# Kernel tuning notes

Measured on AMD Instinct MI355X. Metric: run time of the kernel, lower is better.

## Reference

```python
import jax, jax.numpy as jnp
import numpy as np

T, B, D, H, L = 512, 128, 400, 400, 3


def setup_inputs() -> dict:
    key = jax.random.key(0)
    ks = jax.random.split(key, 12)
    x = jax.random.normal(ks[0], (T, B, D), dtype=jnp.float32)
    lengths = jnp.sort(jax.random.randint(ks[1], (B,), 1, T + 1))[::-1]
    s = 1.0 / np.sqrt(H)
    def w(k, shape):
        return jax.random.normal(k, shape, dtype=jnp.float32) * s
    return {
        "x": x,
        "lengths": lengths,
        # forward-direction cells: layer0 input D, layers 1..2 input 2H
        "Wih_f0": w(ks[2], (4 * H, D)),
        "Wih_f12": w(ks[3], (L - 1, 4 * H, 2 * H)),
        "Whh_f": w(ks[4], (L, 4 * H, H)),
        "b_f": jnp.zeros((L, 4 * H), jnp.float32),
        # backward-direction cells
        "Wih_b0": w(ks[5], (4 * H, D)),
        "Wih_b12": w(ks[6], (L - 1, 4 * H, 2 * H)),
        "Whh_b": w(ks[7], (L, 4 * H, H)),
        "b_b": jnp.zeros((L, 4 * H), jnp.float32),
    }


def _layer(x, mask, Wih, Whh, bias, reverse):
    # x: [T,B,Din], mask: [T,B] bool. Precompute input-side gates once.
    gx = jnp.einsum("tbd,gd->tbg", x, Wih) + bias  # [T,B,4H]
    nb, h_dim = x.shape[1], Whh.shape[-1]

    def step(carry, inp):
        h, c = carry
        g_x, m = inp
        g = g_x + h @ Whh.T
        i, f, gc, o = jnp.split(g, 4, axis=-1)
        i, f, o = jax.nn.sigmoid(i), jax.nn.sigmoid(f), jax.nn.sigmoid(o)
        gc = jnp.tanh(gc)
        c_new = f * c + i * gc
        h_new = o * jnp.tanh(c_new)
        m = m[:, None]
        # inactive sequences keep old state (fwd) / init zeros (bwd) -- matches packed semantics
        h = jnp.where(m, h_new, h)
        c = jnp.where(m, c_new, c)
        return (h, c), h

    if reverse:
        gx, m_seq = gx[::-1], mask[::-1]
    else:
        m_seq = mask
    init = (jnp.zeros((nb, h_dim), x.dtype), jnp.zeros((nb, h_dim), x.dtype))
    _, out = jax.lax.scan(step, init, (gx, m_seq))
    if reverse:
        out = out[::-1]
    return out * mask[:, :, None]


def reference(x, lengths, Wih_f0, Wih_f12, Whh_f, b_f, Wih_b0, Wih_b12, Whh_b, b_b):
    mask = jnp.arange(x.shape[0])[:, None] < lengths[None, :]  # [T,B]
    Wih_fs = [Wih_f0, Wih_f12[0], Wih_f12[1]]
    Wih_bs = [Wih_b0, Wih_b12[0], Wih_b12[1]]
    for l in range(L):
        f = _layer(x, mask, Wih_fs[l], Whh_f[l], b_f[l], reverse=False)
        b = _layer(x, mask, Wih_bs[l], Whh_b[l], b_b[l], reverse=True)
        x = jnp.concatenate([f, b], axis=-1)  # [T,B,2H]
    return x
```

## Files before the change

kernel.cpp:

```cpp
#include <hip/hip_runtime.h>
#include <stdint.h>
#include <stddef.h>

#define T_ 512
#define B_ 128
#define D_ 400
#define H_ 400
#define HP 416
#define GP 1664
#define NW 3328
#define K0P 448
#define K12P 832
#define NTILES 13
#define NGRP 8
#define REC_BLOCKS 208
#define PAIRS 208

#define GC_FSTRIDE 576

#define HBT_U64   ((size_t)16*2*16*PAIRS)
#define HBT_BYTES (HBT_U64*8)

#define WHHR_US8  ((size_t)2*13*4*2*13*64)
#define WHHR_BYTES (WHHR_US8*8*2)

typedef __attribute__((ext_vector_type(8))) __bf16 bf16x8;
typedef __attribute__((ext_vector_type(4))) float f32x4;
typedef __attribute__((ext_vector_type(8))) unsigned short us8;

__device__ __forceinline__ unsigned short f2bf(float f){
  unsigned u = __builtin_bit_cast(unsigned, f);
  u = (u + 0x7FFFu + ((u >> 16) & 1u)) >> 16;
  return (unsigned short)u;
}
__device__ __forceinline__ float bf2f(unsigned short s){
  unsigned u = ((unsigned)s) << 16;
  return __builtin_bit_cast(float, u);
}
__device__ __forceinline__ float sigm(float x){ return 1.f / (1.f + __expf(-x)); }
__device__ __forceinline__ float tanh_f(float x){
  float ax = fabsf(x);
  float e = __expf(-2.f * ax);
  float t = (1.f - e) / (1.f + e);
  return x < 0.f ? -t : t;
}
__device__ __forceinline__ void store_gx(float* p, float v){ *p = v; }
__device__ __forceinline__ void store_gx(unsigned short* p, float v){ *p = f2bf(v); }

__device__ __forceinline__ void h_store_u64(unsigned long long* p, unsigned long long v){
  __hip_atomic_store(p, v, __ATOMIC_RELAXED, __HIP_MEMORY_SCOPE_AGENT);
}
__device__ __forceinline__ unsigned long long h_load_u64(const unsigned long long* p){
  return __hip_atomic_load(p, __ATOMIC_RELAXED, __HIP_MEMORY_SCOPE_AGENT);
}

__global__ void k_conv_x0(const float* __restrict__ x, unsigned short* __restrict__ xa){
  const size_t i = (size_t)blockIdx.x*256 + threadIdx.x;
  if (i >= (size_t)T_*B_*K0P) return;
  const int k = (int)(i % K0P);
  const size_t tb = i / K0P;
  xa[i] = f2bf(k < D_ ? x[tb*D_ + k] : 0.f);
}

__global__ void k_prep_wih(const float* __restrict__ wf, const float* __restrict__ wb,
                           int K, int mode, unsigned short* __restrict__ dst){
  const size_t i = (size_t)blockIdx.x*256 + threadIdx.x;
  if (i >= (size_t)NW*K) return;
  const int k = (int)(i % K);
  const int n = (int)(i / K);
  const int d = n / GP, ng = n % GP, g = ng / HP, r = ng % HP;
  const float* Wsrc = d ? wb : wf;
  float v = 0.f;
  if (r < H_){
    if (mode == 0){
      if (k < D_) v = Wsrc[(size_t)(g*H_ + r)*D_ + k];
    } else {
      int ks = (k < 400) ? k : ((k >= 416 && k < 816) ? (k - 16) : -1);
      if (ks >= 0) v = Wsrc[(size_t)(g*H_ + r)*800 + ks];
    }
  }
  dst[i] = f2bf(v);
}

__global__ void k_prep_whhR(const float* __restrict__ wf, const float* __restrict__ wb,
                            unsigned short* __restrict__ dst){
  const size_t i = (size_t)blockIdx.x*256 + threadIdx.x;
  if (i >= WHHR_US8) return;
  const int lane = (int)(i & 63);
  size_t q = i >> 6;
  const int kk = (int)(q % 13); q /= 13;
  const int ch = (int)(q % 2);  q /= 2;
  const int w  = (int)(q % 4);  q /= 4;
  const int tile = (int)(q % 13);
  const int dirx = (int)(q / 13);
  const int c  = tile*32 + ch*16 + (lane & 15);
  const int k0 = kk*32 + (lane >> 4)*8;
  const float* W = dirx ? wb : wf;
  unsigned short v[8];
  #pragma unroll
  for (int e = 0; e < 8; ++e){
    const int k = k0 + e;
    const float x = (c < H_ && k < H_) ? W[(size_t)(w*H_ + c)*H_ + k] : 0.f;
    v[e] = f2bf(x);
  }
  *(us8*)(dst + i*8) = *(const us8*)v;
}

__global__ void k_prep_bias(const float* __restrict__ bsf, const float* __restrict__ bsb,
                            float* __restrict__ dst){
  const int n = blockIdx.x*256 + threadIdx.x;
  if (n >= NW) return;
  const int d = n / GP, ng = n % GP, g = ng / HP, r = ng % HP;
  dst[n] = (r < H_) ? (d ? bsb : bsf)[g*H_ + r] : 0.f;
}

template<typename GXT>
__global__ __launch_bounds__(256) void gemm_gx(
    const unsigned short* __restrict__ X, int lda, int K,
    const unsigned short* __restrict__ W,
    const float* __restrict__ bias,
    GXT* __restrict__ gx,
    const int* __restrict__ lens)
{
  const int t = blockIdx.y;
  if (t >= lens[0]) return;
  const int n0 = blockIdx.x * 128;
  __shared__ unsigned short As[128*64];
  __shared__ unsigned short Bs[128*64];
  const int tid = threadIdx.x;
  const int l = tid & 63;
  const int w = tid >> 6;
  const int wm = (w >> 1) * 64, wn = (w & 1) * 64;
  const int lr = l & 15, lk = l >> 4;
  f32x4 acc[4][4];
  #pragma unroll
  for (int i = 0; i < 4; ++i)
    #pragma unroll
    for (int j = 0; j < 4; ++j) acc[i][j] = (f32x4){0.f,0.f,0.f,0.f};

  const unsigned short* Xb = X + (size_t)t * B_ * lda;
  const int r_ = tid >> 3, s_ = (tid & 7) * 8;

  for (int k0 = 0; k0 < K; k0 += 64){
    us8 va[4], vb[4];
    #pragma unroll
    for (int i = 0; i < 4; ++i){
      const int r = i*32 + r_;
      va[i] = *(const us8*)(Xb + (size_t)r*lda + k0 + s_);
      vb[i] = *(const us8*)(W  + (size_t)(n0 + r)*K + k0 + s_);
    }
    __syncthreads();
    #pragma unroll
    for (int i = 0; i < 4; ++i){
      const int r = i*32 + r_;
      *(us8*)&As[r*64 + s_] = va[i];
      *(us8*)&Bs[r*64 + s_] = vb[i];
    }
    __syncthreads();
    #pragma unroll
    for (int kk = 0; kk < 2; ++kk){
      bf16x8 af[4], bfr[4];
      #pragma unroll
      for (int mi = 0; mi < 4; ++mi)
        af[mi] = __builtin_bit_cast(bf16x8, *(const us8*)&As[(wm + mi*16 + lr)*64 + kk*32 + lk*8]);
      #pragma unroll
      for (int ni = 0; ni < 4; ++ni)
        bfr[ni] = __builtin_bit_cast(bf16x8, *(const us8*)&Bs[(wn + ni*16 + lr)*64 + kk*32 + lk*8]);
      #pragma unroll
      for (int mi = 0; mi < 4; ++mi)
        #pragma unroll
        for (int ni = 0; ni < 4; ++ni)
          acc[mi][ni] = __builtin_amdgcn_mfma_f32_16x16x32_bf16(af[mi], bfr[ni], acc[mi][ni], 0, 0, 0);
    }
  }
  #pragma unroll
  for (int ni = 0; ni < 4; ++ni){
    const int col = n0 + wn + ni*16 + lr;
    const float bv = bias[col];
    #pragma unroll
    for (int mi = 0; mi < 4; ++mi){
      #pragma unroll
      for (int r = 0; r < 4; ++r){
        const int b = wm + mi*16 + lk*4 + r;
        store_gx(gx + ((size_t)t*B_ + b)*NW + col, acc[mi][ni][r] + bv);
      }
    }
  }
}

template<typename GXT, bool LAST>
__global__ __launch_bounds__(256, 1) void lstm_rec(
    const GXT* __restrict__ gx,
    const unsigned short* __restrict__ whhR,
    const int* __restrict__ lens,
    unsigned long long* hbt,
    unsigned short* __restrict__ xn,
    float* __restrict__ out)
{
  __shared__ unsigned short HS[16*424];
  __shared__ float GC[4*GC_FSTRIDE];
  __shared__ float GXS[16*132];

  const int tid = threadIdx.x;
  const int bid = blockIdx.x;
  const int dir  = bid / 104;
  const int rem  = bid % 104;
  const int grp  = rem / NTILES;
  const int tile = rem % NTILES;
  const int l  = tid & 63;
  const int w  = tid >> 6;
  const int lr = l & 15;
  const int lk = l >> 4;
  const int cid = dir*NGRP + grp;

  us8 Bf0[13], Bf1[13];
  {
    const unsigned short* bs =
        whhR + ((size_t)((dir*13 + tile)*4 + w)*2*13*64 + l)*8;
    #pragma unroll
    for (int kk = 0; kk < 13; ++kk)
      Bf0[kk] = *(const us8*)(bs + (size_t)kk*512);
    const unsigned short* bs1 = bs + (size_t)13*64*8;
    #pragma unroll
    for (int kk = 0; kk < 13; ++kk)
      Bf1[kk] = *(const us8*)(bs1 + (size_t)kk*512);
  }
  const int grp_len = lens[grp*16];
  const int eb  = tid & 15;
  const int p2  = tid >> 4;
  const int mylen = lens[grp*16 + eb];
  float cs0 = 0.f, cs1 = 0.f, hs0 = 0.f, hs1 = 0.f;
  __syncthreads();

  int s_a = 0;
  const int pb = tid >> 4, q = tid & 15, qg = q >> 2, qj = (q & 3) * 8;
  unsigned long long* const myslot =
      hbt + (((size_t)cid*2)*16 + eb)*PAIRS + tile*16 + p2;

  for (int s = 0; s < T_; ++s){
    const int t = dir ? (T_ - 1 - s) : s;
    if (t >= grp_len) continue;

    f32x4 pfa, pfb;
    {
      const size_t goff = ((size_t)t*B_ + grp*16 + pb) * NW + (size_t)dir*GP + qg*HP + tile*32 + qj;
      if constexpr (sizeof(GXT) == 4){
        const float* gp = (const float*)gx + goff;
        pfa = *(const f32x4*)gp;
        pfb = *(const f32x4*)(gp + 4);
      } else {
        us8 v = *(const us8*)((const unsigned short*)gx + goff);
        pfa = (f32x4){bf2f(v[0]), bf2f(v[1]), bf2f(v[2]), bf2f(v[3])};
        pfb = (f32x4){bf2f(v[4]), bf2f(v[5]), bf2f(v[6]), bf2f(v[7])};
      }
    }

    {
      const unsigned rtag = (unsigned)s_a;
      const unsigned long long* hb =
          hbt + ((size_t)(cid*2 + (s_a & 1))*16)*PAIRS;
      unsigned long long v[13];
      #pragma unroll
      for (int j = 0; j < 13; ++j)
        v[j] = h_load_u64(hb + j*256 + tid);
      unsigned stale = 0;
      #pragma unroll
      for (int j = 0; j < 13; ++j)
        if ((unsigned)(v[j] >> 32) != rtag) stale |= 1u << j;
      while (stale){
        const unsigned m = stale;
        #pragma unroll
        for (int j = 0; j < 13; ++j)
          if (m & (1u << j)) v[j] = h_load_u64(hb + j*256 + tid);
        #pragma unroll
        for (int j = 0; j < 13; ++j)
          if ((m & (1u << j)) && (unsigned)(v[j] >> 32) == rtag) stale &= ~(1u << j);
      }
      #pragma unroll
      for (int j = 0; j < 13; ++j){
        const int idx = j*256 + tid;
        const int b = idx / PAIRS, p = idx % PAIRS;
        *(unsigned*)&HS[b*424 + 2*p] = (unsigned)v[j];
      }
    }
    __syncthreads();

    f32x4 a0 = (f32x4){0.f,0.f,0.f,0.f}, a1 = (f32x4){0.f,0.f,0.f,0.f};
    {
      const int ab = lr*424 + lk*8;
      #pragma unroll
      for (int kk = 0; kk < 13; ++kk){
        bf16x8 av = __builtin_bit_cast(bf16x8, *(const us8*)&HS[ab + kk*32]);
        a0 = __builtin_amdgcn_mfma_f32_16x16x32_bf16(av, Bf0[kk], a0, 0, 0, 0);
        a1 = __builtin_amdgcn_mfma_f32_16x16x32_bf16(av, Bf1[kk], a1, 0, 0, 0);
      }
    }
    {
      float* Gw = GC + w * GC_FSTRIDE;
      #pragma unroll
      for (int r = 0; r < 4; ++r){
        Gw[(lk*4 + r)*36 + lr]      = a0[r];
        Gw[(lk*4 + r)*36 + 16 + lr] = a1[r];
      }
      float* gp = GXS + pb*132 + qg*32 + qj;
      *(f32x4*)gp = pfa;
      *(f32x4*)(gp + 4) = pfb;
    }
    __syncthreads();

    const bool act = t < mylen;
    const int c0 = 2*p2, c1 = 2*p2 + 1;
    {
      const float gi0 = GC[0*GC_FSTRIDE + eb*36 + c0] + GXS[eb*132 + c0];
      const float gf0 = GC[1*GC_FSTRIDE + eb*36 + c0] + GXS[eb*132 + 32 + c0];
      const float gg0 = GC[2*GC_FSTRIDE + eb*36 + c0] + GXS[eb*132 + 64 + c0];
      const float go0 = GC[3*GC_FSTRIDE + eb*36 + c0] + GXS[eb*132 + 96 + c0];
      const float gi1 = GC[0*GC_FSTRIDE + eb*36 + c1] + GXS[eb*132 + c1];
      const float gf1 = GC[1*GC_FSTRIDE + eb*36 + c1] + GXS[eb*132 + 32 + c1];
      const float gg1 = GC[2*GC_FSTRIDE + eb*36 + c1] + GXS[eb*132 + 64 + c1];
      const float go1 = GC[3*GC_FSTRIDE + eb*36 + c1] + GXS[eb*132 + 96 + c1];
      const float cn0 = sigm(gf0)*cs0 + sigm(gi0)*tanh_f(gg0);
      const float hn0 = sigm(go0) * tanh_f(cn0);
      const float cn1 = sigm(gf1)*cs1 + sigm(gi1)*tanh_f(gg1);
      const float hn1 = sigm(go1) * tanh_f(cn1);
      if (act){ cs0 = cn0; hs0 = hn0; cs1 = cn1; hs1 = hn1; }
    }
    {
      const unsigned hu = (unsigned)f2bf(hs0) | ((unsigned)f2bf(hs1) << 16);
      const unsigned long long hv =
          (unsigned long long)hu | ((unsigned long long)(unsigned)(s_a + 1) << 32);
      h_store_u64(myslot + ((size_t)((s_a + 1) & 1))*16*PAIRS, hv);
    }
    if (act){
      const int bg = grp*16 + eb;
      const int hc = tile*32 + c0;
      if constexpr (LAST){
        float* op = out + ((size_t)t*B_ + bg)*800 + dir*H_ + hc;
        if (hc < H_)     op[0] = hs0;
        if (hc + 1 < H_) op[1] = hs1;
      } else {
        const unsigned hu = (unsigned)f2bf(hs0) | ((unsigned)f2bf(hs1) << 16);
        *(unsigned*)(xn + ((size_t)t*B_ + bg)*832 + (size_t)dir*HP + hc) = hu;
      }
    }
    ++s_a;
  }
}

template<typename GXT>
static void run_all(void* const* din, float* out, char* ws, hipStream_t stream)
{
  const float* x      = (const float*)din[0];
  const int* lens     = (const int*)din[1];
  const float* wihf0  = (const float*)din[2];
  const float* wihf12 = (const float*)din[3];
  const float* whhf   = (const float*)din[4];
  const float* bsf    = (const float*)din[5];
  const float* wihb0  = (const float*)din[6];
  const float* wihb12 = (const float*)din[7];
  const float* whhb   = (const float*)din[8];
  const float* bsb    = (const float*)din[9];

  char* p = ws;
  auto alloc = [&](size_t n){ char* r = p; p += (n + 255) & ~(size_t)255; return r; };
  GXT* gx            = (GXT*)alloc((size_t)T_*B_*NW*sizeof(GXT));
  unsigned short* xA = (unsigned short*)alloc((size_t)T_*B_*832*2);
  unsigned short* xB = (unsigned short*)alloc((size_t)T_*B_*832*2);
  unsigned short* wihp = (unsigned short*)alloc((size_t)NW*K12P*2);
  unsigned short* whhR = (unsigned short*)alloc(WHHR_BYTES);
  float* biasp       = (float*)alloc((size_t)NW*4);
  unsigned long long* hbt = (unsigned long long*)alloc(HBT_BYTES);

  hipMemsetAsync(out, 0, (size_t)T_*B_*800*4, stream);
  {
    size_t n = (size_t)T_*B_*K0P;
    k_conv_x0<<<dim3((unsigned)((n+255)/256)), dim3(256), 0, stream>>>(x, xA);
  }

  const unsigned short* xin[3] = {xA, xB, xA};
  unsigned short* xout[3] = {xB, xA, nullptr};
  const int ldas[3] = {K0P, 832, 832};
  const int Ks[3]   = {K0P, K12P, K12P};

  for (int lyr = 0; lyr < 3; ++lyr){
    const float* wf = (lyr == 0) ? wihf0 : wihf12 + (size_t)(lyr-1)*1600*800;
    const float* wb = (lyr == 0) ? wihb0 : wihb12 + (size_t)(lyr-1)*1600*800;
    {
      size_t n = (size_t)NW*Ks[lyr];
      k_prep_wih<<<dim3((unsigned)((n+255)/256)), dim3(256), 0, stream>>>(
          wf, wb, Ks[lyr], lyr ? 1 : 0, wihp);
    }
    k_prep_bias<<<dim3((NW+255)/256), dim3(256), 0, stream>>>(
        bsf + (size_t)lyr*1600, bsb + (size_t)lyr*1600, biasp);
    gemm_gx<GXT><<<dim3(26, 512), dim3(256), 0, stream>>>(
        xin[lyr], ldas[lyr], Ks[lyr], wihp, biasp, gx, lens);
    {
      size_t n = WHHR_US8;
      k_prep_whhR<<<dim3((unsigned)((n+255)/256)), dim3(256), 0, stream>>>(
          whhf + (size_t)lyr*1600*400, whhb + (size_t)lyr*1600*400, whhR);
    }
    hipMemsetAsync(hbt, 0, HBT_BYTES, stream);

    const GXT* a_gx = gx;
    const unsigned short* a_whhR = whhR;
    const int* a_lens = lens;
    unsigned long long* a_hbt = hbt;
    unsigned short* a_xn = xout[lyr];
    float* a_out = out;
    void* args[6] = {&a_gx, &a_whhR, &a_lens, &a_hbt, &a_xn, &a_out};
    if (lyr < 2)
      hipLaunchCooperativeKernel(reinterpret_cast<const void*>(&lstm_rec<GXT,false>),
                                 dim3(REC_BLOCKS), dim3(256), args, 0, stream);
    else
      hipLaunchCooperativeKernel(reinterpret_cast<const void*>(&lstm_rec<GXT,true>),
                                 dim3(REC_BLOCKS), dim3(256), args, 0, stream);
  }
}

extern "C" void kernel_launch(void* const* d_in, const int* in_sizes, int n_in,
                              void* d_out, int out_size, void* d_ws, size_t ws_size,
                              hipStream_t stream)
{
  (void)in_sizes; (void)n_in; (void)out_size;
  auto align = [](size_t n){ return (n + 255) & ~(size_t)255; };
  const size_t fixed =
      align((size_t)T_*B_*832*2) * 2 +
      align((size_t)NW*K12P*2) +
      align(WHHR_BYTES) +
      align((size_t)NW*4) +
      align(HBT_BYTES);
  const size_t need32 = align((size_t)T_*B_*NW*4) + fixed;
  const size_t need16 = align((size_t)T_*B_*NW*2) + fixed;

  if (ws_size >= need32)
    run_all<float>(d_in, (float*)d_out, (char*)d_ws, stream);
  else if (ws_size >= need16)
    run_all<unsigned short>(d_in, (float*)d_out, (char*)d_ws, stream);
  else
    hipMemsetAsync(d_out, 0, (size_t)T_*B_*800*4, stream);
}
```

Baseline: 6.368 ms.

## Fuse all four LSTM gates per wave to drop the shared-memory gate exchange

The recurrent kernel now runs 128 threads (2 waves) per block. Each wave holds the Whh fragments for all four gates of its 16 columns (52 register fragments), so the cell update is applied straight from the MFMA accumulators. This removes the GC shared-memory staging buffer and one block barrier per step. The h exchange buffer switches to per-element 32-bit slots, each carrying a 16-bit step tag, read back as tagged u64 pairs, and the cooperative launch becomes a plain launch. In exchange there is heavy register pressure, half the waves per block, and a plain launch that no longer guarantees all 208 spinning blocks are co-resident.

```diff
diff --git a/kernel.cpp b/kernel.cpp
--- a/kernel.cpp
+++ b/kernel.cpp
@@ -14,12 +14,9 @@
 #define NTILES 13
 #define NGRP 8
 #define REC_BLOCKS 208
-#define PAIRS 208
-
-#define GC_FSTRIDE 576
-
-#define HBT_U64   ((size_t)16*2*16*PAIRS)
-#define HBT_BYTES (HBT_U64*8)
+
+#define HBT_U32   ((size_t)16*2*16*416)
+#define HBT_BYTES (HBT_U32*4)
 
 #define WHHR_US8  ((size_t)2*13*4*2*13*64)
 #define WHHR_BYTES (WHHR_US8*8*2)
@@ -47,7 +44,7 @@
 __device__ __forceinline__ void store_gx(float* p, float v){ *p = v; }
 __device__ __forceinline__ void store_gx(unsigned short* p, float v){ *p = f2bf(v); }
 
-__device__ __forceinline__ void h_store_u64(unsigned long long* p, unsigned long long v){
+__device__ __forceinline__ void h_store_u32(unsigned* p, unsigned v){
   __hip_atomic_store(p, v, __ATOMIC_RELAXED, __HIP_MEMORY_SCOPE_AGENT);
 }
 __device__ __forceinline__ unsigned long long h_load_u64(const unsigned long long* p){
@@ -189,160 +186,165 @@
 }
 
 template<typename GXT, bool LAST>
-__global__ __launch_bounds__(256, 1) void lstm_rec(
+__global__ __launch_bounds__(128, 1) void lstm_rec(
     const GXT* __restrict__ gx,
     const unsigned short* __restrict__ whhR,
     const int* __restrict__ lens,
-    unsigned long long* hbt,
+    unsigned int* hbt,
     unsigned short* __restrict__ xn,
     float* __restrict__ out)
 {
   __shared__ unsigned short HS[16*424];
-  __shared__ float GC[4*GC_FSTRIDE];
   __shared__ float GXS[16*132];
 
   const int tid = threadIdx.x;
+  const int cf = tid >> 6, l = tid & 63;
+  const int li = l & 15, lq = l >> 4;
   const int bid = blockIdx.x;
   const int dir  = bid / 104;
   const int rem  = bid % 104;
   const int grp  = rem / NTILES;
   const int tile = rem % NTILES;
-  const int l  = tid & 63;
-  const int w  = tid >> 6;
-  const int lr = l & 15;
-  const int lk = l >> 4;
   const int cid = dir*NGRP + grp;
 
-  us8 Bf0[13], Bf1[13];
-  {
+  us8 Bf[52];
+  #pragma unroll
+  for (int g = 0; g < 4; ++g){
     const unsigned short* bs =
-        whhR + ((size_t)((dir*13 + tile)*4 + w)*2*13*64 + l)*8;
+        whhR + ((size_t)(((dir*13 + tile)*4 + g)*2 + cf)*13*64 + l)*8;
     #pragma unroll
     for (int kk = 0; kk < 13; ++kk)
-      Bf0[kk] = *(const us8*)(bs + (size_t)kk*512);
-    const unsigned short* bs1 = bs + (size_t)13*64*8;
-    #pragma unroll
-    for (int kk = 0; kk < 13; ++kk)
-      Bf1[kk] = *(const us8*)(bs1 + (size_t)kk*512);
-  }
+      Bf[g*13 + kk] = *(const us8*)(bs + (size_t)kk*512);
+  }
+  unsigned hsOff[26];
+  #pragma unroll
+  for (int j = 0; j < 26; ++j){
+    const int idx = j*128 + tid;
+    const int b = idx / 208, cp = idx % 208;
+    hsOff[j] = (unsigned)(b*424 + 2*cp);
+  }
+
   const int grp_len = lens[grp*16];
-  const int eb  = tid & 15;
-  const int p2  = tid >> 4;
-  const int mylen = lens[grp*16 + eb];
-  float cs0 = 0.f, cs1 = 0.f, hs0 = 0.f, hs1 = 0.f;
+  int len_r[4];
+  #pragma unroll
+  for (int r = 0; r < 4; ++r) len_r[r] = lens[grp*16 + lq*4 + r];
+  float cs[4] = {0.f,0.f,0.f,0.f}, hs[4] = {0.f,0.f,0.f,0.f};
   __syncthreads();
 
   int s_a = 0;
-  const int pb = tid >> 4, q = tid & 15, qg = q >> 2, qj = (q & 3) * 8;
-  unsigned long long* const myslot =
-      hbt + (((size_t)cid*2)*16 + eb)*PAIRS + tile*16 + p2;
+  const int pb = tid >> 3, q2 = tid & 7;
+  const int qg = q2 >> 1, qh = (q2 & 1)*16;
+  const int myc = tile*32 + cf*16 + li;
 
   for (int s = 0; s < T_; ++s){
     const int t = dir ? (T_ - 1 - s) : s;
     if (t >= grp_len) continue;
 
-    f32x4 pfa, pfb;
-    {
-      const size_t goff = ((size_t)t*B_ + grp*16 + pb) * NW + (size_t)dir*GP + qg*HP + tile*32 + qj;
+    f32x4 gv[4];
+    {
+      const size_t goff = ((size_t)t*B_ + grp*16 + pb)*NW
+                        + (size_t)dir*GP + qg*HP + tile*32 + qh;
       if constexpr (sizeof(GXT) == 4){
-        const float* gp = (const float*)gx + goff;
-        pfa = *(const f32x4*)gp;
-        pfb = *(const f32x4*)(gp + 4);
+        const float* fp = (const float*)gx + goff;
+        #pragma unroll
+        for (int u = 0; u < 4; ++u) gv[u] = *(const f32x4*)(fp + u*4);
       } else {
-        us8 v = *(const us8*)((const unsigned short*)gx + goff);
-        pfa = (f32x4){bf2f(v[0]), bf2f(v[1]), bf2f(v[2]), bf2f(v[3])};
-        pfb = (f32x4){bf2f(v[4]), bf2f(v[5]), bf2f(v[6]), bf2f(v[7])};
-      }
-    }
-
-    {
-      const unsigned rtag = (unsigned)s_a;
-      const unsigned long long* hb =
-          hbt + ((size_t)(cid*2 + (s_a & 1))*16)*PAIRS;
-      unsigned long long v[13];
-      #pragma unroll
-      for (int j = 0; j < 13; ++j)
-        v[j] = h_load_u64(hb + j*256 + tid);
+        const unsigned short* up = (const unsigned short*)gx + goff;
+        us8 a0 = *(const us8*)up, a1 = *(const us8*)(up + 8);
+        #pragma unroll
+        for (int e = 0; e < 4; ++e){
+          gv[0][e] = bf2f(a0[e]);   gv[1][e] = bf2f(a0[e+4]);
+          gv[2][e] = bf2f(a1[e]);   gv[3][e] = bf2f(a1[e+4]);
+        }
+      }
+    }
+
+    {
+      const unsigned rtag = (unsigned)(s_a & 0xFFFF);
+      const unsigned long long* hb = (const unsigned long long*)
+          (hbt + (size_t)(cid*2 + (s_a & 1))*16*416);
+      unsigned long long v[26];
+      #pragma unroll
+      for (int j = 0; j < 26; ++j)
+        v[j] = h_load_u64(hb + j*128 + tid);
       unsigned stale = 0;
       #pragma unroll
-      for (int j = 0; j < 13; ++j)
-        if ((unsigned)(v[j] >> 32) != rtag) stale |= 1u << j;
+      for (int j = 0; j < 26; ++j){
+        const unsigned tl = ((unsigned)(v[j] >> 16)) & 0xFFFFu;
+        const unsigned th = (unsigned)(v[j] >> 48);
+        if ((tl != rtag) | (th != rtag)) stale |= 1u << j;
+      }
       while (stale){
         const unsigned m = stale;
         #pragma unroll
-        for (int j = 0; j < 13; ++j)
-          if (m & (1u << j)) v[j] = h_load_u64(hb + j*256 + tid);
+        for (int j = 0; j < 26; ++j)
+          if (m & (1u << j)) v[j] = h_load_u64(hb + j*128 + tid);
         #pragma unroll
-        for (int j = 0; j < 13; ++j)
-          if ((m & (1u << j)) && (unsigned)(v[j] >> 32) == rtag) stale &= ~(1u << j);
-      }
-      #pragma unroll
-      for (int j = 0; j < 13; ++j){
-        const int idx = j*256 + tid;
-        const int b = idx / PAIRS, p = idx % PAIRS;
-        *(unsigned*)&HS[b*424 + 2*p] = (unsigned)v[j];
-      }
+        for (int j = 0; j < 26; ++j){
+          if (m & (1u << j)){
+            const unsigned tl = ((unsigned)(v[j] >> 16)) & 0xFFFFu;
+            const unsigned th = (unsigned)(v[j] >> 48);
+            if ((tl == rtag) & (th == rtag)) stale &= ~(1u << j);
+          }
+        }
+      }
+      #pragma unroll
+      for (int j = 0; j < 26; ++j){
+        const unsigned pk = ((unsigned)v[j] & 0xFFFFu)
+                          | (((unsigned)(v[j] >> 32) & 0xFFFFu) << 16);
+        *(unsigned*)&HS[hsOff[j]] = pk;
+      }
+    }
+    {
+      float* gp = &GXS[pb*132 + qg*32 + qh];
+      *(f32x4*)gp        = gv[0];
+      *(f32x4*)(gp + 4)  = gv[1];
+      *(f32x4*)(gp + 8)  = gv[2];
+      *(f32x4*)(gp + 12) = gv[3];
     }
     __syncthreads();
 
-    f32x4 a0 = (f32x4){0.f,0.f,0.f,0.f}, a1 = (f32x4){0.f,0.f,0.f,0.f};
-    {
-      const int ab = lr*424 + lk*8;
+    f32x4 acc[4];
+    #pragma unroll
+    for (int g = 0; g < 4; ++g) acc[g] = (f32x4){0.f,0.f,0.f,0.f};
+    {
+      const int ab = li*424 + lq*8;
       #pragma unroll
       for (int kk = 0; kk < 13; ++kk){
-        bf16x8 av = __builtin_bit_cast(bf16x8, *(const us8*)&HS[ab + kk*32]);
-        a0 = __builtin_amdgcn_mfma_f32_16x16x32_bf16(av, Bf0[kk], a0, 0, 0, 0);
-        a1 = __builtin_amdgcn_mfma_f32_16x16x32_bf16(av, Bf1[kk], a1, 0, 0, 0);
-      }
-    }
-    {
-      float* Gw = GC + w * GC_FSTRIDE;
-      #pragma unroll
-      for (int r = 0; r < 4; ++r){
-        Gw[(lk*4 + r)*36 + lr]      = a0[r];
-        Gw[(lk*4 + r)*36 + 16 + lr] = a1[r];
-      }
-      float* gp = GXS + pb*132 + qg*32 + qj;
-      *(f32x4*)gp = pfa;
-      *(f32x4*)(gp + 4) = pfb;
+        const bf16x8 av = __builtin_bit_cast(bf16x8, *(const us8*)&HS[ab + kk*32]);
+        acc[0] = __builtin_amdgcn_mfma_f32_16x16x32_bf16(av, Bf[     kk], acc[0], 0, 0, 0);
+        acc[1] = __builtin_amdgcn_mfma_f32_16x16x32_bf16(av, Bf[13 + kk], acc[1], 0, 0, 0);
+        acc[2] = __builtin_amdgcn_mfma_f32_16x16x32_bf16(av, Bf[26 + kk], acc[2], 0, 0, 0);
+        acc[3] = __builtin_amdgcn_mfma_f32_16x16x32_bf16(av, Bf[39 + kk], acc[3], 0, 0, 0);
+      }
+    }
+
+    unsigned* hbW = hbt + (size_t)(cid*2 + ((s_a + 1) & 1))*16*416;
+    const unsigned tagw = ((unsigned)((s_a + 1) & 0xFFFF)) << 16;
+    #pragma unroll
+    for (int r = 0; r < 4; ++r){
+      const int bb = lq*4 + r;
+      const float gi = acc[0][r] + GXS[bb*132 +        cf*16 + li];
+      const float gf = acc[1][r] + GXS[bb*132 +  32 + cf*16 + li];
+      const float gg = acc[2][r] + GXS[bb*132 +  64 + cf*16 + li];
+      const float go = acc[3][r] + GXS[bb*132 +  96 + cf*16 + li];
+      const float cn = sigm(gf)*cs[r] + sigm(gi)*tanh_f(gg);
+      const float hn = sigm(go) * tanh_f(cn);
+      if (t < len_r[r]){ cs[r] = cn; hs[r] = hn; }
+      h_store_u32(hbW + (size_t)bb*416 + myc, (unsigned)f2bf(hs[r]) | tagw);
+    }
+    #pragma unroll
+    for (int r = 0; r < 4; ++r){
+      if (t < len_r[r]){
+        const int bg = grp*16 + lq*4 + r;
+        if constexpr (LAST){
+          if (myc < H_) out[((size_t)t*B_ + bg)*800 + dir*H_ + myc] = hs[r];
+        } else {
+          xn[((size_t)t*B_ + bg)*832 + (size_t)dir*HP + myc] = f2bf(hs[r]);
+        }
+      }
     }
     __syncthreads();
-
-    const bool act = t < mylen;
-    const int c0 = 2*p2, c1 = 2*p2 + 1;
-    {
-      const float gi0 = GC[0*GC_FSTRIDE + eb*36 + c0] + GXS[eb*132 + c0];
-      const float gf0 = GC[1*GC_FSTRIDE + eb*36 + c0] + GXS[eb*132 + 32 + c0];
-      const float gg0 = GC[2*GC_FSTRIDE + eb*36 + c0] + GXS[eb*132 + 64 + c0];
-      const float go0 = GC[3*GC_FSTRIDE + eb*36 + c0] + GXS[eb*132 + 96 + c0];
-      const float gi1 = GC[0*GC_FSTRIDE + eb*36 + c1] + GXS[eb*132 + c1];
-      const float gf1 = GC[1*GC_FSTRIDE + eb*36 + c1] + GXS[eb*132 + 32 + c1];
-      const float gg1 = GC[2*GC_FSTRIDE + eb*36 + c1] + GXS[eb*132 + 64 + c1];
-      const float go1 = GC[3*GC_FSTRIDE + eb*36 + c1] + GXS[eb*132 + 96 + c1];
-      const float cn0 = sigm(gf0)*cs0 + sigm(gi0)*tanh_f(gg0);
-      const float hn0 = sigm(go0) * tanh_f(cn0);
-      const float cn1 = sigm(gf1)*cs1 + sigm(gi1)*tanh_f(gg1);
-      const float hn1 = sigm(go1) * tanh_f(cn1);
-      if (act){ cs0 = cn0; hs0 = hn0; cs1 = cn1; hs1 = hn1; }
-    }
-    {
-      const unsigned hu = (unsigned)f2bf(hs0) | ((unsigned)f2bf(hs1) << 16);
-      const unsigned long long hv =
-          (unsigned long long)hu | ((unsigned long long)(unsigned)(s_a + 1) << 32);
-      h_store_u64(myslot + ((size_t)((s_a + 1) & 1))*16*PAIRS, hv);
-    }
-    if (act){
-      const int bg = grp*16 + eb;
-      const int hc = tile*32 + c0;
-      if constexpr (LAST){
-        float* op = out + ((size_t)t*B_ + bg)*800 + dir*H_ + hc;
-        if (hc < H_)     op[0] = hs0;
-        if (hc + 1 < H_) op[1] = hs1;
-      } else {
-        const unsigned hu = (unsigned)f2bf(hs0) | ((unsigned)f2bf(hs1) << 16);
-        *(unsigned*)(xn + ((size_t)t*B_ + bg)*832 + (size_t)dir*HP + hc) = hu;
-      }
-    }
     ++s_a;
   }
 }
@@ -369,7 +371,7 @@
   unsigned short* wihp = (unsigned short*)alloc((size_t)NW*K12P*2);
   unsigned short* whhR = (unsigned short*)alloc(WHHR_BYTES);
   float* biasp       = (float*)alloc((size_t)NW*4);
-  unsigned long long* hbt = (unsigned long long*)alloc(HBT_BYTES);
+  unsigned int* hbt  = (unsigned int*)alloc(HBT_BYTES);
 
   hipMemsetAsync(out, 0, (size_t)T_*B_*800*4, stream);
   {
@@ -401,19 +403,12 @@
     }
     hipMemsetAsync(hbt, 0, HBT_BYTES, stream);
 
-    const GXT* a_gx = gx;
-    const unsigned short* a_whhR = whhR;
-    const int* a_lens = lens;
-    unsigned long long* a_hbt = hbt;
-    unsigned short* a_xn = xout[lyr];
-    float* a_out = out;
-    void* args[6] = {&a_gx, &a_whhR, &a_lens, &a_hbt, &a_xn, &a_out};
     if (lyr < 2)
-      hipLaunchCooperativeKernel(reinterpret_cast<const void*>(&lstm_rec<GXT,false>),
-                                 dim3(REC_BLOCKS), dim3(256), args, 0, stream);
+      lstm_rec<GXT,false><<<dim3(REC_BLOCKS), dim3(128), 0, stream>>>(
+          gx, whhR, lens, hbt, xout[lyr], out);
     else
-      hipLaunchCooperativeKernel(reinterpret_cast<const void*>(&lstm_rec<GXT,true>),
-                                 dim3(REC_BLOCKS), dim3(256), args, 0, stream);
+      lstm_rec<GXT,true><<<dim3(REC_BLOCKS), dim3(128), 0, stream>>>(
+          gx, whhR, lens, hbt, nullptr, out);
   }
 }
 
```

Result: slower. 8.298 ms (+30.3%).

## Prefetch next-step gates and hidden-state loads, iterate only active steps, use plain launch

Applied to the files above, without the earlier changes.

The recurrent LSTM kernel now issues the global loads for the next timestep's input gates and the exchanged hidden-state slots right after the MFMA phase. These loads land in a double-buffered shared GXS array and in registers, which hides their latency behind the gate math. The loop runs only grp_len steps instead of iterating all T steps and skipping inactive ones. The cooperative launch is replaced with an ordinary launch, which relies on all 208 blocks being co-resident for the spin-wait exchange. Early hidden-state loads may read stale tags more often and trigger extra polling, and shared memory use grows.

```diff
diff --git a/kernel.cpp b/kernel.cpp
--- a/kernel.cpp
+++ b/kernel.cpp
@@ -199,7 +199,7 @@
 {
   __shared__ unsigned short HS[16*424];
   __shared__ float GC[4*GC_FSTRIDE];
-  __shared__ float GXS[16*132];
+  __shared__ float GXS[2*16*132];
 
   const int tid = threadIdx.x;
   const int bid = blockIdx.x;
@@ -232,37 +232,38 @@
   float cs0 = 0.f, cs1 = 0.f, hs0 = 0.f, hs1 = 0.f;
   __syncthreads();
 
-  int s_a = 0;
   const int pb = tid >> 4, q = tid & 15, qg = q >> 2, qj = (q & 3) * 8;
   unsigned long long* const myslot =
       hbt + (((size_t)cid*2)*16 + eb)*PAIRS + tile*16 + p2;
 
-  for (int s = 0; s < T_; ++s){
-    const int t = dir ? (T_ - 1 - s) : s;
-    if (t >= grp_len) continue;
-
-    f32x4 pfa, pfb;
-    {
-      const size_t goff = ((size_t)t*B_ + grp*16 + pb) * NW + (size_t)dir*GP + qg*HP + tile*32 + qj;
-      if constexpr (sizeof(GXT) == 4){
-        const float* gp = (const float*)gx + goff;
-        pfa = *(const f32x4*)gp;
-        pfb = *(const f32x4*)(gp + 4);
-      } else {
-        us8 v = *(const us8*)((const unsigned short*)gx + goff);
-        pfa = (f32x4){bf2f(v[0]), bf2f(v[1]), bf2f(v[2]), bf2f(v[3])};
-        pfb = (f32x4){bf2f(v[4]), bf2f(v[5]), bf2f(v[6]), bf2f(v[7])};
-      }
-    }
-
-    {
-      const unsigned rtag = (unsigned)s_a;
-      const unsigned long long* hb =
-          hbt + ((size_t)(cid*2 + (s_a & 1))*16)*PAIRS;
-      unsigned long long v[13];
-      #pragma unroll
-      for (int j = 0; j < 13; ++j)
-        v[j] = h_load_u64(hb + j*256 + tid);
+  const int nsteps = grp_len;
+  f32x4 pfa, pfb;
+  unsigned long long v[13];
+
+  {
+    const int t0 = dir ? (grp_len - 1) : 0;
+    const size_t goff = ((size_t)t0*B_ + grp*16 + pb) * NW + (size_t)dir*GP + qg*HP + tile*32 + qj;
+    if constexpr (sizeof(GXT) == 4){
+      const float* gp = (const float*)gx + goff;
+      pfa = *(const f32x4*)gp;
+      pfb = *(const f32x4*)(gp + 4);
+    } else {
+      us8 vv = *(const us8*)((const unsigned short*)gx + goff);
+      pfa = (f32x4){bf2f(vv[0]), bf2f(vv[1]), bf2f(vv[2]), bf2f(vv[3])};
+      pfb = (f32x4){bf2f(vv[4]), bf2f(vv[5]), bf2f(vv[6]), bf2f(vv[7])};
+    }
+    const unsigned long long* hb0 = hbt + ((size_t)(cid*2 + 0)*16)*PAIRS;
+    #pragma unroll
+    for (int j = 0; j < 13; ++j)
+      v[j] = h_load_u64(hb0 + j*256 + tid);
+  }
+
+  for (int ss = 0; ss < nsteps; ++ss){
+    const int t = dir ? (grp_len - 1 - ss) : ss;
+
+    {
+      const unsigned rtag = (unsigned)ss;
+      const unsigned long long* hb = hbt + ((size_t)(cid*2 + (ss & 1))*16)*PAIRS;
       unsigned stale = 0;
       #pragma unroll
       for (int j = 0; j < 13; ++j)
@@ -283,6 +284,11 @@
         *(unsigned*)&HS[b*424 + 2*p] = (unsigned)v[j];
       }
     }
+    {
+      float* gp = GXS + (ss & 1)*2112 + pb*132 + qg*32 + qj;
+      *(f32x4*)gp = pfa;
+      *(f32x4*)(gp + 4) = pfb;
+    }
     __syncthreads();
 
     f32x4 a0 = (f32x4){0.f,0.f,0.f,0.f}, a1 = (f32x4){0.f,0.f,0.f,0.f};
@@ -302,23 +308,38 @@
         Gw[(lk*4 + r)*36 + lr]      = a0[r];
         Gw[(lk*4 + r)*36 + 16 + lr] = a1[r];
       }
-      float* gp = GXS + pb*132 + qg*32 + qj;
-      *(f32x4*)gp = pfa;
-      *(f32x4*)(gp + 4) = pfb;
+    }
+    if (ss + 1 < nsteps){
+      const int tn = dir ? (grp_len - 2 - ss) : (ss + 1);
+      const size_t goff = ((size_t)tn*B_ + grp*16 + pb) * NW + (size_t)dir*GP + qg*HP + tile*32 + qj;
+      if constexpr (sizeof(GXT) == 4){
+        const float* gp = (const float*)gx + goff;
+        pfa = *(const f32x4*)gp;
+        pfb = *(const f32x4*)(gp + 4);
+      } else {
+        us8 vv = *(const us8*)((const unsigned short*)gx + goff);
+        pfa = (f32x4){bf2f(vv[0]), bf2f(vv[1]), bf2f(vv[2]), bf2f(vv[3])};
+        pfb = (f32x4){bf2f(vv[4]), bf2f(vv[5]), bf2f(vv[6]), bf2f(vv[7])};
+      }
+      const unsigned long long* hbn = hbt + ((size_t)(cid*2 + ((ss + 1) & 1))*16)*PAIRS;
+      #pragma unroll
+      for (int j = 0; j < 13; ++j)
+        v[j] = h_load_u64(hbn + j*256 + tid);
     }
     __syncthreads();
 
     const bool act = t < mylen;
     const int c0 = 2*p2, c1 = 2*p2 + 1;
     {
-      const float gi0 = GC[0*GC_FSTRIDE + eb*36 + c0] + GXS[eb*132 + c0];
-      const float gf0 = GC[1*GC_FSTRIDE + eb*36 + c0] + GXS[eb*132 + 32 + c0];
-      const float gg0 = GC[2*GC_FSTRIDE + eb*36 + c0] + GXS[eb*132 + 64 + c0];
-      const float go0 = GC[3*GC_FSTRIDE + eb*36 + c0] + GXS[eb*132 + 96 + c0];
-      const float gi1 = GC[0*GC_FSTRIDE + eb*36 + c1] + GXS[eb*132 + c1];
-      const float gf1 = GC[1*GC_FSTRIDE + eb*36 + c1] + GXS[eb*132 + 32 + c1];
-      const float gg1 = GC[2*GC_FSTRIDE + eb*36 + c1] + GXS[eb*132 + 64 + c1];
-      const float go1 = GC[3*GC_FSTRIDE + eb*36 + c1] + GXS[eb*132 + 96 + c1];
+      const float* GXp = GXS + (ss & 1)*2112;
+      const float gi0 = GC[0*GC_FSTRIDE + eb*36 + c0] + GXp[eb*132 + c0];
+      const float gf0 = GC[1*GC_FSTRIDE + eb*36 + c0] + GXp[eb*132 + 32 + c0];
+      const float gg0 = GC[2*GC_FSTRIDE + eb*36 + c0] + GXp[eb*132 + 64 + c0];
+      const float go0 = GC[3*GC_FSTRIDE + eb*36 + c0] + GXp[eb*132 + 96 + c0];
+      const float gi1 = GC[0*GC_FSTRIDE + eb*36 + c1] + GXp[eb*132 + c1];
+      const float gf1 = GC[1*GC_FSTRIDE + eb*36 + c1] + GXp[eb*132 + 32 + c1];
+      const float gg1 = GC[2*GC_FSTRIDE + eb*36 + c1] + GXp[eb*132 + 64 + c1];
+      const float go1 = GC[3*GC_FSTRIDE + eb*36 + c1] + GXp[eb*132 + 96 + c1];
       const float cn0 = sigm(gf0)*cs0 + sigm(gi0)*tanh_f(gg0);
       const float hn0 = sigm(go0) * tanh_f(cn0);
       const float cn1 = sigm(gf1)*cs1 + sigm(gi1)*tanh_f(gg1);
@@ -328,8 +349,8 @@
     {
       const unsigned hu = (unsigned)f2bf(hs0) | ((unsigned)f2bf(hs1) << 16);
       const unsigned long long hv =
-          (unsigned long long)hu | ((unsigned long long)(unsigned)(s_a + 1) << 32);
-      h_store_u64(myslot + ((size_t)((s_a + 1) & 1))*16*PAIRS, hv);
+          (unsigned long long)hu | ((unsigned long long)(unsigned)(ss + 1) << 32);
+      h_store_u64(myslot + ((size_t)((ss + 1) & 1))*16*PAIRS, hv);
     }
     if (act){
       const int bg = grp*16 + eb;
@@ -343,7 +364,6 @@
         *(unsigned*)(xn + ((size_t)t*B_ + bg)*832 + (size_t)dir*HP + hc) = hu;
       }
     }
-    ++s_a;
   }
 }
 
@@ -401,19 +421,12 @@
     }
     hipMemsetAsync(hbt, 0, HBT_BYTES, stream);
 
-    const GXT* a_gx = gx;
-    const unsigned short* a_whhR = whhR;
-    const int* a_lens = lens;
-    unsigned long long* a_hbt = hbt;
-    unsigned short* a_xn = xout[lyr];
-    float* a_out = out;
-    void* args[6] = {&a_gx, &a_whhR, &a_lens, &a_hbt, &a_xn, &a_out};
     if (lyr < 2)
-      hipLaunchCooperativeKernel(reinterpret_cast<const void*>(&lstm_rec<GXT,false>),
-                                 dim3(REC_BLOCKS), dim3(256), args, 0, stream);
+      lstm_rec<GXT,false><<<dim3(REC_BLOCKS), dim3(256), 0, stream>>>(
+          gx, whhR, lens, hbt, xout[lyr], out);
     else
-      hipLaunchCooperativeKernel(reinterpret_cast<const void*>(&lstm_rec<GXT,true>),
-                                 dim3(REC_BLOCKS), dim3(256), args, 0, stream);
+      lstm_rec<GXT,true><<<dim3(REC_BLOCKS), dim3(256), 0, stream>>>(
+          gx, whhR, lens, hbt, nullptr, out);
   }
 }
 
```

New measurement: 6.612 ms. +3.8%, slower.
